# Optimization experiments

Measured on AMD Instinct MI355X. Metric: run time of the kernel, lower is better.

Reference implementation:

```python
import jax, jax.numpy as jnp
import numpy as np
from jax import lax

WIN = 9
LOSS_WEIGHT = 1.0

def _box_sum(x, win):
    return lax.reduce_window(x, 0.0, lax.add,
                             window_dimensions=(1, 1, win, win, win),
                             window_strides=(1, 1, 1, 1, 1),
                             padding='SAME')

def setup_inputs() -> dict:
    key = jax.random.key(0)
    k1, k2 = jax.random.split(key)
    shape = (2, 1, 160, 192, 160)
    predict = jax.random.uniform(k1, shape, dtype=jnp.float32)
    target = jax.random.uniform(k2, shape, dtype=jnp.float32)
    return {"predict": predict, "target": target}

def reference(predict, target):
    Ii, Ji = target, predict
    win = WIN
    win_size = float(win ** 3)

    I_sum = _box_sum(Ii, win)
    J_sum = _box_sum(Ji, win)
    I2_sum = _box_sum(Ii * Ii, win)
    J2_sum = _box_sum(Ji * Ji, win)
    IJ_sum = _box_sum(Ii * Ji, win)

    u_I = I_sum / win_size
    u_J = J_sum / win_size
    cross = IJ_sum - u_J * I_sum - u_I * J_sum + u_I * u_J * win_size
    I_var = I2_sum - 2.0 * u_I * I_sum + u_I * u_I * win_size
    J_var = J2_sum - 2.0 * u_J * J_sum + u_J * u_J * win_size
    cc = cross * cross / (I_var * J_var + 1e-05)
    loss = 1.0 - jnp.mean(cc)
    return loss * LOSS_WEIGHT
```

## Files before the change

kernel.cpp:

```cpp
#include <hip/hip_runtime.h>
#include <hip/hip_fp16.h>


#define NX 160
#define NY 192
#define NZ 160
#define NB 2
#define SLICE (NX * NY)
#define VOL   (SLICE * NZ)
#define TOTAL (VOL * NB)

#define TX 32
#define TY 16
#define ZC 8
#define GXT (NX / TX)
#define GYT (NY / TY)
#define GZT (NZ / ZC)
#define NBLK (GXT * GYT * GZT * NB)

#define HY 24
#define ZRS 56
#define ZQQ (HY * ZRS + 8)
#define RRS 40
#define RQQ (HY * RRS + 8)
#define SRS 40
#define SQQ (TY * SRS + 8)
#define INV729 (1.0f / 729.0f)

__device__ __forceinline__ void lds_barrier() {
    asm volatile("s_waitcnt lgkmcnt(0)" ::: "memory");
    __builtin_amdgcn_s_barrier();
}

__device__ __forceinline__ float4 f4add(float4 a, float4 b) {
    return make_float4(a.x + b.x, a.y + b.y, a.z + b.z, a.w + b.w);
}
__device__ __forceinline__ float4 f4sub(float4 a, float4 b) {
    return make_float4(a.x - b.x, a.y - b.y, a.z - b.z, a.w - b.w);
}
__device__ __forceinline__ float4 f4mul(float4 a, float4 b) {
    return make_float4(a.x * b.x, a.y * b.y, a.z * b.z, a.w * b.w);
}

union U8 { uint4 u; __half2 h[4]; };

__device__ __forceinline__ U8 ld8(const __half* p) {
    U8 r; r.u = *(const uint4*)p; return r;
}
__device__ __forceinline__ void st8(__half* p, const U8& v) {
    *(uint4*)p = v.u;
}

__global__ __launch_bounds__(256) void ncc_main(
    const float* __restrict__ J_pred,
    const float* __restrict__ I_targ,
    float* __restrict__ partial)
{
    const int tid = threadIdx.x;

    const int lin = blockIdx.x;
    const int s   = (lin & 7) * (NBLK / 8) + (lin >> 3);
    const int bx  = s % GXT;
    const int r1  = s / GXT;
    const int by  = r1 % GYT;
    const int r2  = r1 / GYT;
    const int zc  = r2 % GZT;
    const int b   = r2 / GZT;

    const int x0 = bx * TX;
    const int y0 = by * TY;
    const int z0 = zc * ZC;

    __shared__ __align__(16) __half Zq[5 * ZQQ];
    __shared__ __align__(16) __half Rq[5 * RQQ];
    __shared__ float redbuf[4];
    __half* const Sq = Zq;

    const bool is_col = (tid < 240);
    const int  crow = tid / 10;
    const int  cxg  = tid - crow * 10;
    const int  gy = y0 - 4 + crow;
    const int  gx = x0 - 4 + cxg * 4;
    const bool vxy = is_col && ((unsigned)gy < (unsigned)NY) && (gx >= 0) && (gx <= NX - 4);
    const size_t cbase = (size_t)b * VOL + (vxy ? (size_t)(gy * NX + gx) : 0);
    const float* const baseI = I_targ + cbase;
    const float* const baseJ = J_pred + cbase;

    const float4 f40 = make_float4(0.f, 0.f, 0.f, 0.f);
    float4 rS0 = f40, rS1 = f40, rS2 = f40, rS3 = f40, rS4 = f40;

#pragma unroll 3
    for (int ss = 0; ss < 9; ++ss) {
        const int z = z0 - 5 + ss;
        float4 aI = f40, aJ = f40;
        if (vxy && (unsigned)z < (unsigned)NZ) {
            aI = *(const float4*)(baseI + (size_t)z * SLICE);
            aJ = *(const float4*)(baseJ + (size_t)z * SLICE);
        }
        rS0 = f4add(rS0, aI);
        rS1 = f4add(rS1, aJ);
        rS2 = f4add(rS2, f4mul(aI, aI));
        rS3 = f4add(rS3, f4mul(aJ, aJ));
        rS4 = f4add(rS4, f4mul(aI, aJ));
    }

    float4 nIa = f40, nJa = f40, nIs = f40, nJs = f40;
    if (vxy) {
        const int za = z0 + 4;
        nIa = *(const float4*)(baseI + (size_t)za * SLICE);
        nJa = *(const float4*)(baseJ + (size_t)za * SLICE);
        const int zs = z0 - 5;
        if (zs >= 0) {
            nIs = *(const float4*)(baseI + (size_t)zs * SLICE);
            nJs = *(const float4*)(baseJ + (size_t)zs * SLICE);
        }
    }

    const int ty  = tid >> 4;
    const int tx2 = tid & 15;
    float acc = 0.f;

#pragma unroll 1
    for (int so = 0; so < ZC; ++so) {
        rS0 = f4add(rS0, f4sub(nIa, nIs));
        rS1 = f4add(rS1, f4sub(nJa, nJs));
        rS2 = f4add(rS2, f4sub(f4mul(nIa, nIa), f4mul(nIs, nIs)));
        rS3 = f4add(rS3, f4sub(f4mul(nJa, nJa), f4mul(nJs, nJs)));
        rS4 = f4add(rS4, f4sub(f4mul(nIa, nJa), f4mul(nIs, nJs)));

        nIa = f40; nJa = f40; nIs = f40; nJs = f40;
        if (so < ZC - 1 && vxy) {
            const int za = z0 + 5 + so;
            if (za < NZ) {
                nIa = *(const float4*)(baseI + (size_t)za * SLICE);
                nJa = *(const float4*)(baseJ + (size_t)za * SLICE);
            }
            const int zs = z0 + so - 4;
            if (zs >= 0) {
                nIs = *(const float4*)(baseI + (size_t)zs * SLICE);
                nJs = *(const float4*)(baseJ + (size_t)zs * SLICE);
            }
        }

        if (is_col) {
            const int o = crow * ZRS + cxg * 4;
            union { uint2 u; __half2 h[2]; } pk;
            pk.h[0] = __float22half2_rn(make_float2(rS0.x, rS0.y));
            pk.h[1] = __float22half2_rn(make_float2(rS0.z, rS0.w));
            *(uint2*)&Zq[0 * ZQQ + o] = pk.u;
            pk.h[0] = __float22half2_rn(make_float2(rS1.x, rS1.y));
            pk.h[1] = __float22half2_rn(make_float2(rS1.z, rS1.w));
            *(uint2*)&Zq[1 * ZQQ + o] = pk.u;
            pk.h[0] = __float22half2_rn(make_float2(rS2.x, rS2.y));
            pk.h[1] = __float22half2_rn(make_float2(rS2.z, rS2.w));
            *(uint2*)&Zq[2 * ZQQ + o] = pk.u;
            pk.h[0] = __float22half2_rn(make_float2(rS3.x, rS3.y));
            pk.h[1] = __float22half2_rn(make_float2(rS3.z, rS3.w));
            *(uint2*)&Zq[3 * ZQQ + o] = pk.u;
            pk.h[0] = __float22half2_rn(make_float2(rS4.x, rS4.y));
            pk.h[1] = __float22half2_rn(make_float2(rS4.z, rS4.w));
            *(uint2*)&Zq[4 * ZQQ + o] = pk.u;
        }
        lds_barrier();

        if (tid < 240) {
            const int q   = tid / 48;
            const int rem = tid - q * 48;
            const int row = rem >> 1;
            const int h   = rem & 1;
            const __half* src = &Zq[q * ZQQ + row * ZRS + h * 16];
            float c[24];
#pragma unroll
            for (int g = 0; g < 3; ++g) {
                U8 v = ld8(src + g * 8);
#pragma unroll
                for (int j = 0; j < 4; ++j) {
                    const float2 f = __half22float2(v.h[j]);
                    c[g * 8 + j * 2 + 0] = f.x;
                    c[g * 8 + j * 2 + 1] = f.y;
                }
            }
            float sx = c[0] + c[1] + c[2] + c[3] + c[4]
                     + c[5] + c[6] + c[7] + c[8];
            float o[16];
            o[0] = sx;
#pragma unroll
            for (int i = 1; i < 16; ++i) { sx += c[i + 8] - c[i - 1]; o[i] = sx; }
            __half* dst = &Rq[q * RQQ + row * RRS + h * 16];
#pragma unroll
            for (int g = 0; g < 2; ++g) {
                U8 w;
#pragma unroll
                for (int j = 0; j < 4; ++j)
                    w.h[j] = __float22half2_rn(make_float2(o[g * 8 + j * 2],
                                                           o[g * 8 + j * 2 + 1]));
                st8(dst + g * 8, w);
            }
        }
        lds_barrier();

        if (tid < 80) {
            const int q  = tid / 16;
            const int rm = tid & 15;
            const int xg = rm >> 2;
            const int q4 = rm & 3;
            const __half* rb = &Rq[q * RQQ + (q4 * 4) * RRS + xg * 8];
            __half* sb = &Sq[q * SQQ + (q4 * 4) * SRS + xg * 8];
            U8 sum = ld8(rb);
#pragma unroll
            for (int k = 1; k < 9; ++k) {
                const U8 t = ld8(rb + k * RRS);
#pragma unroll
                for (int j = 0; j < 4; ++j) sum.h[j] = __hadd2(sum.h[j], t.h[j]);
            }
            st8(sb, sum);
#pragma unroll
            for (int i = 1; i < 4; ++i) {
                const U8 nw = ld8(rb + (i + 8) * RRS);
                const U8 od = ld8(rb + (i - 1) * RRS);
#pragma unroll
                for (int j = 0; j < 4; ++j)
                    sum.h[j] = __hadd2(sum.h[j], __hsub2(nw.h[j], od.h[j]));
                st8(sb + i * SRS, sum);
            }
        }
        lds_barrier();

        {
            const int o = ty * SRS + tx2 * 2;
            const float2 S0 = __half22float2(*(const __half2*)&Sq[0 * SQQ + o]);
            const float2 S1 = __half22float2(*(const __half2*)&Sq[1 * SQQ + o]);
            const float2 S2 = __half22float2(*(const __half2*)&Sq[2 * SQQ + o]);
            const float2 S3 = __half22float2(*(const __half2*)&Sq[3 * SQQ + o]);
            const float2 S4 = __half22float2(*(const __half2*)&Sq[4 * SQQ + o]);
            {
                const float cross = S4.x - S0.x * S1.x * INV729;
                const float Iv    = S2.x - S0.x * S0.x * INV729;
                const float Jv    = S3.x - S1.x * S1.x * INV729;
                acc += (cross * cross) / (Iv * Jv + 1e-5f);
            }
            {
                const float cross = S4.y - S0.y * S1.y * INV729;
                const float Iv    = S2.y - S0.y * S0.y * INV729;
                const float Jv    = S3.y - S1.y * S1.y * INV729;
                acc += (cross * cross) / (Iv * Jv + 1e-5f);
            }
        }
        lds_barrier();
    }

#pragma unroll
    for (int off = 32; off > 0; off >>= 1) acc += __shfl_down(acc, off);
    __syncthreads();
    if ((tid & 63) == 0) redbuf[tid >> 6] = acc;
    __syncthreads();
    if (tid == 0) partial[s] = redbuf[0] + redbuf[1] + redbuf[2] + redbuf[3];
}

__global__ __launch_bounds__(256) void ncc_final(
    const float* __restrict__ partial, float* __restrict__ out)
{
    __shared__ float sm[256];
    const int tid = threadIdx.x;
    float v = 0.f;
    for (int i = tid; i < NBLK; i += 256) v += partial[i];
    sm[tid] = v;
    __syncthreads();
#pragma unroll
    for (int w = 128; w > 0; w >>= 1) {
        if (tid < w) sm[tid] += sm[tid + w];
        __syncthreads();
    }
    if (tid == 0) out[0] = 1.0f - sm[0] * (1.0f / (float)TOTAL);
}

extern "C" void kernel_launch(void* const* d_in, const int* in_sizes, int n_in,
                              void* d_out, int out_size, void* d_ws, size_t ws_size,
                              hipStream_t stream)
{
    const float* predict = (const float*)d_in[0];
    const float* target  = (const float*)d_in[1];
    float* partial = (float*)d_ws;

    ncc_main<<<dim3(NBLK), 256, 0, stream>>>(predict, target, partial);
    ncc_final<<<1, 256, 0, stream>>>(partial, (float*)d_out);
}
```

Before: 60.62 us.

## Use single-wavefront blocks with 16x16 tiles to drop workgroup barriers

Each block shrinks to one 64-lane wavefront that handles a 16x16 xy tile. Each lane now owns up to three halo columns, and the per-column z running sums are kept in registers. Because the block is a single wave, the s_barrier calls between LDS stages are replaced by lgkmcnt waits only, which removes workgroup synchronisation cost. In exchange the halo overhead per tile rises (24x24 halo for 16x16 outputs), which means more redundant global loads and more blocks. Register pressure also goes up from the 3x5 float4 running sums, and the loads are no longer prefetched a step ahead.

```diff
diff --git a/kernel.cpp b/kernel.cpp
--- a/kernel.cpp
+++ b/kernel.cpp
@@ -10,7 +10,7 @@
 #define VOL   (SLICE * NZ)
 #define TOTAL (VOL * NB)
 
-#define TX 32
+#define TX 16
 #define TY 16
 #define ZC 8
 #define GXT (NX / TX)
@@ -18,18 +18,17 @@
 #define GZT (NZ / ZC)
 #define NBLK (GXT * GYT * GZT * NB)
 
-#define HY 24
-#define ZRS 56
-#define ZQQ (HY * ZRS + 8)
-#define RRS 40
-#define RQQ (HY * RRS + 8)
-#define SRS 40
-#define SQQ (TY * SRS + 8)
+#define HR 24
+#define ZQS 24
+#define ZQQ (HR * ZQS + 8)
+#define RQS 24
+#define RQQ (HR * RQS + 8)
+#define SQS 16
+#define SQQ (TY * SQS + 8)
 #define INV729 (1.0f / 729.0f)
 
-__device__ __forceinline__ void lds_barrier() {
+__device__ __forceinline__ void lds_fence() {
     asm volatile("s_waitcnt lgkmcnt(0)" ::: "memory");
-    __builtin_amdgcn_s_barrier();
 }
 
 __device__ __forceinline__ float4 f4add(float4 a, float4 b) {
@@ -43,7 +42,6 @@
 }
 
 union U8 { uint4 u; __half2 h[4]; };
-
 __device__ __forceinline__ U8 ld8(const __half* p) {
     U8 r; r.u = *(const uint4*)p; return r;
 }
@@ -51,12 +49,12 @@
     *(uint4*)p = v.u;
 }
 
-__global__ __launch_bounds__(256) void ncc_main(
+__global__ __launch_bounds__(64) void ncc_main(
     const float* __restrict__ J_pred,
     const float* __restrict__ I_targ,
     float* __restrict__ partial)
 {
-    const int tid = threadIdx.x;
+    const int lane = threadIdx.x;
 
     const int lin = blockIdx.x;
     const int s   = (lin & 7) * (NBLK / 8) + (lin >> 3);
@@ -73,188 +71,195 @@
 
     __shared__ __align__(16) __half Zq[5 * ZQQ];
     __shared__ __align__(16) __half Rq[5 * RQQ];
-    __shared__ float redbuf[4];
-    __half* const Sq = Zq;
-
-    const bool is_col = (tid < 240);
-    const int  crow = tid / 10;
-    const int  cxg  = tid - crow * 10;
-    const int  gy = y0 - 4 + crow;
-    const int  gx = x0 - 4 + cxg * 4;
-    const bool vxy = is_col && ((unsigned)gy < (unsigned)NY) && (gx >= 0) && (gx <= NX - 4);
-    const size_t cbase = (size_t)b * VOL + (vxy ? (size_t)(gy * NX + gx) : 0);
-    const float* const baseI = I_targ + cbase;
-    const float* const baseJ = J_pred + cbase;
+    __shared__ __align__(16) __half Sq[5 * SQQ];
+
+    int  orow[3], oxg[3];
+    bool exist[3], ok[3];
+    const float* bI[3];
+    const float* bJ[3];
+    const size_t bvol = (size_t)b * VOL;
+#pragma unroll
+    for (int r = 0; r < 3; ++r) {
+        const int c = lane + r * 64;
+        exist[r] = (c < 144);
+        const int row = c / 6;
+        const int x   = c - row * 6;
+        orow[r] = row; oxg[r] = x;
+        const int gy = y0 - 4 + row;
+        const int gx = x0 - 4 + x * 4;
+        ok[r] = exist[r] && ((unsigned)gy < (unsigned)NY) && (gx >= 0) && (gx <= NX - 4);
+        const size_t cb = bvol + (ok[r] ? (size_t)(gy * NX + gx) : 0);
+        bI[r] = I_targ + cb;
+        bJ[r] = J_pred + cb;
+    }
 
     const float4 f40 = make_float4(0.f, 0.f, 0.f, 0.f);
-    float4 rS0 = f40, rS1 = f40, rS2 = f40, rS3 = f40, rS4 = f40;
-
-#pragma unroll 3
+    float4 run[3][5];
+#pragma unroll
+    for (int r = 0; r < 3; ++r)
+#pragma unroll
+        for (int q = 0; q < 5; ++q) run[r][q] = f40;
+
+#pragma unroll 1
     for (int ss = 0; ss < 9; ++ss) {
         const int z = z0 - 5 + ss;
-        float4 aI = f40, aJ = f40;
-        if (vxy && (unsigned)z < (unsigned)NZ) {
-            aI = *(const float4*)(baseI + (size_t)z * SLICE);
-            aJ = *(const float4*)(baseJ + (size_t)z * SLICE);
-        }
-        rS0 = f4add(rS0, aI);
-        rS1 = f4add(rS1, aJ);
-        rS2 = f4add(rS2, f4mul(aI, aI));
-        rS3 = f4add(rS3, f4mul(aJ, aJ));
-        rS4 = f4add(rS4, f4mul(aI, aJ));
-    }
-
-    float4 nIa = f40, nJa = f40, nIs = f40, nJs = f40;
-    if (vxy) {
-        const int za = z0 + 4;
-        nIa = *(const float4*)(baseI + (size_t)za * SLICE);
-        nJa = *(const float4*)(baseJ + (size_t)za * SLICE);
-        const int zs = z0 - 5;
-        if (zs >= 0) {
-            nIs = *(const float4*)(baseI + (size_t)zs * SLICE);
-            nJs = *(const float4*)(baseJ + (size_t)zs * SLICE);
-        }
-    }
-
-    const int ty  = tid >> 4;
-    const int tx2 = tid & 15;
+        const bool zok = ((unsigned)z < (unsigned)NZ);
+#pragma unroll
+        for (int r = 0; r < 3; ++r) {
+            float4 aI = f40, aJ = f40;
+            if (ok[r] && zok) {
+                aI = *(const float4*)(bI[r] + (size_t)z * SLICE);
+                aJ = *(const float4*)(bJ[r] + (size_t)z * SLICE);
+            }
+            run[r][0] = f4add(run[r][0], aI);
+            run[r][1] = f4add(run[r][1], aJ);
+            run[r][2] = f4add(run[r][2], f4mul(aI, aI));
+            run[r][3] = f4add(run[r][3], f4mul(aJ, aJ));
+            run[r][4] = f4add(run[r][4], f4mul(aI, aJ));
+        }
+    }
+
+    const int prow = lane >> 2;
+    const int pxq  = (lane & 3) * 4;
     float acc = 0.f;
 
 #pragma unroll 1
     for (int so = 0; so < ZC; ++so) {
-        rS0 = f4add(rS0, f4sub(nIa, nIs));
-        rS1 = f4add(rS1, f4sub(nJa, nJs));
-        rS2 = f4add(rS2, f4sub(f4mul(nIa, nIa), f4mul(nIs, nIs)));
-        rS3 = f4add(rS3, f4sub(f4mul(nJa, nJa), f4mul(nJs, nJs)));
-        rS4 = f4add(rS4, f4sub(f4mul(nIa, nJa), f4mul(nIs, nJs)));
-
-        nIa = f40; nJa = f40; nIs = f40; nJs = f40;
-        if (so < ZC - 1 && vxy) {
-            const int za = z0 + 5 + so;
-            if (za < NZ) {
-                nIa = *(const float4*)(baseI + (size_t)za * SLICE);
-                nJa = *(const float4*)(baseJ + (size_t)za * SLICE);
-            }
-            const int zs = z0 + so - 4;
-            if (zs >= 0) {
-                nIs = *(const float4*)(baseI + (size_t)zs * SLICE);
-                nJs = *(const float4*)(baseJ + (size_t)zs * SLICE);
-            }
-        }
-
-        if (is_col) {
-            const int o = crow * ZRS + cxg * 4;
-            union { uint2 u; __half2 h[2]; } pk;
-            pk.h[0] = __float22half2_rn(make_float2(rS0.x, rS0.y));
-            pk.h[1] = __float22half2_rn(make_float2(rS0.z, rS0.w));
-            *(uint2*)&Zq[0 * ZQQ + o] = pk.u;
-            pk.h[0] = __float22half2_rn(make_float2(rS1.x, rS1.y));
-            pk.h[1] = __float22half2_rn(make_float2(rS1.z, rS1.w));
-            *(uint2*)&Zq[1 * ZQQ + o] = pk.u;
-            pk.h[0] = __float22half2_rn(make_float2(rS2.x, rS2.y));
-            pk.h[1] = __float22half2_rn(make_float2(rS2.z, rS2.w));
-            *(uint2*)&Zq[2 * ZQQ + o] = pk.u;
-            pk.h[0] = __float22half2_rn(make_float2(rS3.x, rS3.y));
-            pk.h[1] = __float22half2_rn(make_float2(rS3.z, rS3.w));
-            *(uint2*)&Zq[3 * ZQQ + o] = pk.u;
-            pk.h[0] = __float22half2_rn(make_float2(rS4.x, rS4.y));
-            pk.h[1] = __float22half2_rn(make_float2(rS4.z, rS4.w));
-            *(uint2*)&Zq[4 * ZQQ + o] = pk.u;
-        }
-        lds_barrier();
-
-        if (tid < 240) {
-            const int q   = tid / 48;
-            const int rem = tid - q * 48;
-            const int row = rem >> 1;
-            const int h   = rem & 1;
-            const __half* src = &Zq[q * ZQQ + row * ZRS + h * 16];
-            float c[24];
-#pragma unroll
-            for (int g = 0; g < 3; ++g) {
-                U8 v = ld8(src + g * 8);
-#pragma unroll
-                for (int j = 0; j < 4; ++j) {
-                    const float2 f = __half22float2(v.h[j]);
-                    c[g * 8 + j * 2 + 0] = f.x;
-                    c[g * 8 + j * 2 + 1] = f.y;
-                }
-            }
-            float sx = c[0] + c[1] + c[2] + c[3] + c[4]
-                     + c[5] + c[6] + c[7] + c[8];
-            float o[16];
-            o[0] = sx;
-#pragma unroll
-            for (int i = 1; i < 16; ++i) { sx += c[i + 8] - c[i - 1]; o[i] = sx; }
-            __half* dst = &Rq[q * RQQ + row * RRS + h * 16];
-#pragma unroll
-            for (int g = 0; g < 2; ++g) {
-                U8 w;
-#pragma unroll
-                for (int j = 0; j < 4; ++j)
-                    w.h[j] = __float22half2_rn(make_float2(o[g * 8 + j * 2],
-                                                           o[g * 8 + j * 2 + 1]));
-                st8(dst + g * 8, w);
-            }
-        }
-        lds_barrier();
-
-        if (tid < 80) {
-            const int q  = tid / 16;
-            const int rm = tid & 15;
+        const int za = z0 + 4 + so;
+        const int zs = z0 + so - 5;
+        const bool zaok = ((unsigned)za < (unsigned)NZ);
+        const bool zsok = (zs >= 0);
+#pragma unroll
+        for (int r = 0; r < 3; ++r) {
+            float4 aI = f40, aJ = f40, sI = f40, sJ = f40;
+            if (ok[r]) {
+                if (zaok) {
+                    aI = *(const float4*)(bI[r] + (size_t)za * SLICE);
+                    aJ = *(const float4*)(bJ[r] + (size_t)za * SLICE);
+                }
+                if (zsok) {
+                    sI = *(const float4*)(bI[r] + (size_t)zs * SLICE);
+                    sJ = *(const float4*)(bJ[r] + (size_t)zs * SLICE);
+                }
+            }
+            run[r][0] = f4add(run[r][0], f4sub(aI, sI));
+            run[r][1] = f4add(run[r][1], f4sub(aJ, sJ));
+            run[r][2] = f4add(run[r][2], f4sub(f4mul(aI, aI), f4mul(sI, sI)));
+            run[r][3] = f4add(run[r][3], f4sub(f4mul(aJ, aJ), f4mul(sJ, sJ)));
+            run[r][4] = f4add(run[r][4], f4sub(f4mul(aI, aJ), f4mul(sI, sJ)));
+        }
+
+#pragma unroll
+        for (int r = 0; r < 3; ++r) {
+            if (exist[r]) {
+                const int o = orow[r] * ZQS + oxg[r] * 4;
+                union { uint2 u; __half2 h[2]; } pk;
+#pragma unroll
+                for (int q = 0; q < 5; ++q) {
+                    pk.h[0] = __float22half2_rn(make_float2(run[r][q].x, run[r][q].y));
+                    pk.h[1] = __float22half2_rn(make_float2(run[r][q].z, run[r][q].w));
+                    *(uint2*)&Zq[q * ZQQ + o] = pk.u;
+                }
+            }
+        }
+        lds_fence();
+
+#pragma unroll
+        for (int rr = 0; rr < 2; ++rr) {
+            const int t = lane + rr * 64;
+            if (t < 120) {
+                const int q   = t / 24;
+                const int row = t - q * 24;
+                const __half* src = &Zq[q * ZQQ + row * ZQS];
+                float c[24];
+#pragma unroll
+                for (int g = 0; g < 3; ++g) {
+                    U8 v = ld8(src + g * 8);
+#pragma unroll
+                    for (int j = 0; j < 4; ++j) {
+                        const float2 f = __half22float2(v.h[j]);
+                        c[g * 8 + j * 2 + 0] = f.x;
+                        c[g * 8 + j * 2 + 1] = f.y;
+                    }
+                }
+                float sx = c[0] + c[1] + c[2] + c[3] + c[4]
+                         + c[5] + c[6] + c[7] + c[8];
+                float o[16];
+                o[0] = sx;
+#pragma unroll
+                for (int i = 1; i < 16; ++i) { sx += c[i + 8] - c[i - 1]; o[i] = sx; }
+                __half* dst = &Rq[q * RQQ + row * RQS];
+#pragma unroll
+                for (int g = 0; g < 2; ++g) {
+                    U8 w;
+#pragma unroll
+                    for (int j = 0; j < 4; ++j)
+                        w.h[j] = __float22half2_rn(make_float2(o[g * 8 + j * 2],
+                                                               o[g * 8 + j * 2 + 1]));
+                    st8(dst + g * 8, w);
+                }
+            }
+        }
+        lds_fence();
+
+        if (lane < 40) {
+            const int q  = lane / 8;
+            const int rm = lane - q * 8;
             const int xg = rm >> 2;
             const int q4 = rm & 3;
-            const __half* rb = &Rq[q * RQQ + (q4 * 4) * RRS + xg * 8];
-            __half* sb = &Sq[q * SQQ + (q4 * 4) * SRS + xg * 8];
+            const __half* rb = &Rq[q * RQQ + (q4 * 4) * RQS + xg * 8];
+            __half* sb = &Sq[q * SQQ + (q4 * 4) * SQS + xg * 8];
             U8 sum = ld8(rb);
 #pragma unroll
             for (int k = 1; k < 9; ++k) {
-                const U8 t = ld8(rb + k * RRS);
+                const U8 t = ld8(rb + k * RQS);
 #pragma unroll
                 for (int j = 0; j < 4; ++j) sum.h[j] = __hadd2(sum.h[j], t.h[j]);
             }
             st8(sb, sum);
 #pragma unroll
             for (int i = 1; i < 4; ++i) {
-                const U8 nw = ld8(rb + (i + 8) * RRS);
-                const U8 od = ld8(rb + (i - 1) * RRS);
+                const U8 nw = ld8(rb + (i + 8) * RQS);
+                const U8 od = ld8(rb + (i - 1) * RQS);
 #pragma unroll
                 for (int j = 0; j < 4; ++j)
                     sum.h[j] = __hadd2(sum.h[j], __hsub2(nw.h[j], od.h[j]));
-                st8(sb + i * SRS, sum);
-            }
-        }
-        lds_barrier();
+                st8(sb + i * SQS, sum);
+            }
+        }
+        lds_fence();
 
         {
-            const int o = ty * SRS + tx2 * 2;
-            const float2 S0 = __half22float2(*(const __half2*)&Sq[0 * SQQ + o]);
-            const float2 S1 = __half22float2(*(const __half2*)&Sq[1 * SQQ + o]);
-            const float2 S2 = __half22float2(*(const __half2*)&Sq[2 * SQQ + o]);
-            const float2 S3 = __half22float2(*(const __half2*)&Sq[3 * SQQ + o]);
-            const float2 S4 = __half22float2(*(const __half2*)&Sq[4 * SQQ + o]);
-            {
-                const float cross = S4.x - S0.x * S1.x * INV729;
-                const float Iv    = S2.x - S0.x * S0.x * INV729;
-                const float Jv    = S3.x - S1.x * S1.x * INV729;
-                acc += (cross * cross) / (Iv * Jv + 1e-5f);
-            }
-            {
-                const float cross = S4.y - S0.y * S1.y * INV729;
-                const float Iv    = S2.y - S0.y * S0.y * INV729;
-                const float Jv    = S3.y - S1.y * S1.y * INV729;
-                acc += (cross * cross) / (Iv * Jv + 1e-5f);
-            }
-        }
-        lds_barrier();
+            const int o = prow * SQS + pxq;
+            union { uint2 u; __half2 h[2]; } v[5];
+#pragma unroll
+            for (int q = 0; q < 5; ++q) v[q].u = *(const uint2*)&Sq[q * SQQ + o];
+#pragma unroll
+            for (int j = 0; j < 2; ++j) {
+                const float2 S0 = __half22float2(v[0].h[j]);
+                const float2 S1 = __half22float2(v[1].h[j]);
+                const float2 S2 = __half22float2(v[2].h[j]);
+                const float2 S3 = __half22float2(v[3].h[j]);
+                const float2 S4 = __half22float2(v[4].h[j]);
+                {
+                    const float cross = S4.x - S0.x * S1.x * INV729;
+                    const float Iv    = S2.x - S0.x * S0.x * INV729;
+                    const float Jv    = S3.x - S1.x * S1.x * INV729;
+                    acc += (cross * cross) / (Iv * Jv + 1e-5f);
+                }
+                {
+                    const float cross = S4.y - S0.y * S1.y * INV729;
+                    const float Iv    = S2.y - S0.y * S0.y * INV729;
+                    const float Jv    = S3.y - S1.y * S1.y * INV729;
+                    acc += (cross * cross) / (Iv * Jv + 1e-5f);
+                }
+            }
+        }
     }
 
 #pragma unroll
     for (int off = 32; off > 0; off >>= 1) acc += __shfl_down(acc, off);
-    __syncthreads();
-    if ((tid & 63) == 0) redbuf[tid >> 6] = acc;
-    __syncthreads();
-    if (tid == 0) partial[s] = redbuf[0] + redbuf[1] + redbuf[2] + redbuf[3];
+    if (lane == 0) partial[s] = acc;
 }
 
 __global__ __launch_bounds__(256) void ncc_final(
@@ -282,6 +287,6 @@
     const float* target  = (const float*)d_in[1];
     float* partial = (float*)d_ws;
 
-    ncc_main<<<dim3(NBLK), 256, 0, stream>>>(predict, target, partial);
+    ncc_main<<<dim3(NBLK), 64, 0, stream>>>(predict, target, partial);
     ncc_final<<<1, 256, 0, stream>>>(partial, (float*)d_out);
 }
```

After: 77.98 us. +28.6%, slower.

## Replace Y-direction box sum and final stage with bf16 MFMA band-matrix multiply

Applied to the files above, without the earlier changes.

The Y-direction 9-tap sliding sum over half-precision rows is replaced by a bf16 MFMA against a constant banded 0/1 weight matrix. The X-pass output is stored as bf16 in a transposed layout and read with ds_read_b64_tr_b16. The NCC epilogue now consumes the MFMA accumulators directly, which removes one LDS stage and one barrier per z-slice. The z-loop is software-pipelined so the MFMA/epilogue of the previous slice overlaps the global loads for the next. Risks include lower bf16 precision in the X-pass sums and only two waves doing the MFMA work.

```diff
diff --git a/kernel.cpp b/kernel.cpp
--- a/kernel.cpp
+++ b/kernel.cpp
@@ -18,20 +18,32 @@
 #define GZT (NZ / ZC)
 #define NBLK (GXT * GYT * GZT * NB)
 
-#define HY 24
-#define ZRS 56
-#define ZQQ (HY * ZRS + 8)
-#define RRS 40
-#define RQQ (HY * RRS + 8)
-#define SRS 40
-#define SQQ (TY * SRS + 8)
+#define HR 24
+#define ZQS 48
+#define ZQQ (HR * ZQS + 8)
+#define RGN 544
 #define INV729 (1.0f / 729.0f)
+
+typedef short bf16x8 __attribute__((ext_vector_type(8)));
+typedef float f32x4 __attribute__((ext_vector_type(4)));
 
 __device__ __forceinline__ void lds_barrier() {
     asm volatile("s_waitcnt lgkmcnt(0)" ::: "memory");
     __builtin_amdgcn_s_barrier();
 }
 
+__device__ __forceinline__ unsigned cvt_pk_bf16(float lo, float hi) {
+    unsigned r;
+    asm("v_cvt_pk_bf16_f32 %0, %1, %2" : "=v"(r) : "v"(lo), "v"(hi));
+    return r;
+}
+
+__device__ __forceinline__ uint2 tr_rd(unsigned a) {
+    uint2 d;
+    asm volatile("ds_read_b64_tr_b16 %0, %1" : "=v"(d) : "v"(a));
+    return d;
+}
+
 __device__ __forceinline__ float4 f4add(float4 a, float4 b) {
     return make_float4(a.x + b.x, a.y + b.y, a.z + b.z, a.w + b.w);
 }
@@ -43,12 +55,8 @@
 }
 
 union U8 { uint4 u; __half2 h[4]; };
-
 __device__ __forceinline__ U8 ld8(const __half* p) {
     U8 r; r.u = *(const uint4*)p; return r;
-}
-__device__ __forceinline__ void st8(__half* p, const U8& v) {
-    *(uint4*)p = v.u;
 }
 
 __global__ __launch_bounds__(256) void ncc_main(
@@ -72,9 +80,14 @@
     const int z0 = zc * ZC;
 
     __shared__ __align__(16) __half Zq[5 * ZQQ];
-    __shared__ __align__(16) __half Rq[5 * RQQ];
+    __shared__ __align__(16) short  RqT[10 * RGN];
     __shared__ float redbuf[4];
-    __half* const Sq = Zq;
+
+    if (tid < 160) {
+        const int r = tid >> 4, slot = tid & 15;
+        const int e = (slot < 8) ? (192 + slot * 8) : (448 + (slot - 8) * 8);
+        *(uint4*)&RqT[r * RGN + e] = make_uint4(0, 0, 0, 0);
+    }
 
     const bool is_col = (tid < 240);
     const int  crow = tid / 10;
@@ -86,10 +99,23 @@
     const float* const baseI = I_targ + cbase;
     const float* const baseJ = J_pred + cbase;
 
+    const int lane = tid & 63;
+    bf16x8 wfrag;
+    {
+        const int m = lane & 15, kb = (lane >> 4) * 8;
+#pragma unroll
+        for (int j = 0; j < 8; ++j) {
+            const int k = kb + j;
+            wfrag[j] = (k >= m && k <= m + 8) ? (short)0x3F80 : (short)0;
+        }
+    }
+    const unsigned rqbase = (unsigned)(size_t)&RqT[0];
+    const unsigned trlane = rqbase + 2u * (unsigned)(lane & 15) + 128u * (unsigned)(lane >> 4);
+
     const float4 f40 = make_float4(0.f, 0.f, 0.f, 0.f);
     float4 rS0 = f40, rS1 = f40, rS2 = f40, rS3 = f40, rS4 = f40;
 
-#pragma unroll 3
+#pragma unroll 1
     for (int ss = 0; ss < 9; ++ss) {
         const int z = z0 - 5 + ss;
         float4 aI = f40, aJ = f40;
@@ -104,46 +130,17 @@
         rS4 = f4add(rS4, f4mul(aI, aJ));
     }
 
-    float4 nIa = f40, nJa = f40, nIs = f40, nJs = f40;
+    float4 nIa = f40, nJa = f40;
     if (vxy) {
-        const int za = z0 + 4;
-        nIa = *(const float4*)(baseI + (size_t)za * SLICE);
-        nJa = *(const float4*)(baseJ + (size_t)za * SLICE);
-        const int zs = z0 - 5;
-        if (zs >= 0) {
-            nIs = *(const float4*)(baseI + (size_t)zs * SLICE);
-            nJs = *(const float4*)(baseJ + (size_t)zs * SLICE);
-        }
-    }
-
-    const int ty  = tid >> 4;
-    const int tx2 = tid & 15;
+        nIa = *(const float4*)(baseI + (size_t)(z0 + 4) * SLICE);
+        nJa = *(const float4*)(baseJ + (size_t)(z0 + 4) * SLICE);
+    }
+
     float acc = 0.f;
 
-#pragma unroll 1
-    for (int so = 0; so < ZC; ++so) {
-        rS0 = f4add(rS0, f4sub(nIa, nIs));
-        rS1 = f4add(rS1, f4sub(nJa, nJs));
-        rS2 = f4add(rS2, f4sub(f4mul(nIa, nIa), f4mul(nIs, nIs)));
-        rS3 = f4add(rS3, f4sub(f4mul(nJa, nJa), f4mul(nJs, nJs)));
-        rS4 = f4add(rS4, f4sub(f4mul(nIa, nJa), f4mul(nIs, nJs)));
-
-        nIa = f40; nJa = f40; nIs = f40; nJs = f40;
-        if (so < ZC - 1 && vxy) {
-            const int za = z0 + 5 + so;
-            if (za < NZ) {
-                nIa = *(const float4*)(baseI + (size_t)za * SLICE);
-                nJa = *(const float4*)(baseJ + (size_t)za * SLICE);
-            }
-            const int zs = z0 + so - 4;
-            if (zs >= 0) {
-                nIs = *(const float4*)(baseI + (size_t)zs * SLICE);
-                nJs = *(const float4*)(baseJ + (size_t)zs * SLICE);
-            }
-        }
-
+    auto do_P1 = [&]() {
         if (is_col) {
-            const int o = crow * ZRS + cxg * 4;
+            const int o = crow * ZQS + cxg * 4;
             union { uint2 u; __half2 h[2]; } pk;
             pk.h[0] = __float22half2_rn(make_float2(rS0.x, rS0.y));
             pk.h[1] = __float22half2_rn(make_float2(rS0.z, rS0.w));
@@ -161,14 +158,15 @@
             pk.h[1] = __float22half2_rn(make_float2(rS4.z, rS4.w));
             *(uint2*)&Zq[4 * ZQQ + o] = pk.u;
         }
-        lds_barrier();
-
+    };
+
+    auto do_P2 = [&]() {
         if (tid < 240) {
             const int q   = tid / 48;
             const int rem = tid - q * 48;
             const int row = rem >> 1;
             const int h   = rem & 1;
-            const __half* src = &Zq[q * ZQQ + row * ZRS + h * 16];
+            const __half* src = &Zq[q * ZQQ + row * ZQS + h * 16];
             float c[24];
 #pragma unroll
             for (int g = 0; g < 3; ++g) {
@@ -186,68 +184,101 @@
             o[0] = sx;
 #pragma unroll
             for (int i = 1; i < 16; ++i) { sx += c[i + 8] - c[i - 1]; o[i] = sx; }
-            __half* dst = &Rq[q * RQQ + row * RRS + h * 16];
-#pragma unroll
-            for (int g = 0; g < 2; ++g) {
-                U8 w;
-#pragma unroll
-                for (int j = 0; j < 4; ++j)
-                    w.h[j] = __float22half2_rn(make_float2(o[g * 8 + j * 2],
-                                                           o[g * 8 + j * 2 + 1]));
-                st8(dst + g * 8, w);
+            unsigned u[8];
+#pragma unroll
+            for (int i = 0; i < 8; ++i) u[i] = cvt_pk_bf16(o[2 * i], o[2 * i + 1]);
+            const int e = 16 * (row & 3) + 64 * (row >> 3) + 256 * ((row >> 2) & 1);
+            short* dst = &RqT[(q * 2 + h) * RGN + e];
+            *(uint4*)(dst + 0) = make_uint4(u[0], u[1], u[2], u[3]);
+            *(uint4*)(dst + 8) = make_uint4(u[4], u[5], u[6], u[7]);
+        }
+    };
+
+    auto do_mfmacc = [&]() {
+        if (tid < 128) {
+            const int h = tid >> 6;
+            const unsigned abase = trlane + (unsigned)h * 1088u;
+            const f32x4 z4 = {0.f, 0.f, 0.f, 0.f};
+            f32x4 D[5];
+#pragma unroll
+            for (int q = 0; q < 5; ++q) {
+                const unsigned a = abase + (unsigned)q * 2176u;
+                uint2 b0 = tr_rd(a);
+                uint2 b1 = tr_rd(a + 512u);
+                asm volatile("s_waitcnt lgkmcnt(0)" ::: "memory");
+                __builtin_amdgcn_sched_barrier(0);
+                union { uint2 u[2]; bf16x8 v; } bb;
+                bb.u[0] = b0; bb.u[1] = b1;
+                D[q] = __builtin_amdgcn_mfma_f32_16x16x32_bf16(wfrag, bb.v, z4, 0, 0, 0);
             }
-        }
-        lds_barrier();
-
-        if (tid < 80) {
-            const int q  = tid / 16;
-            const int rm = tid & 15;
-            const int xg = rm >> 2;
-            const int q4 = rm & 3;
-            const __half* rb = &Rq[q * RQQ + (q4 * 4) * RRS + xg * 8];
-            __half* sb = &Sq[q * SQQ + (q4 * 4) * SRS + xg * 8];
-            U8 sum = ld8(rb);
-#pragma unroll
-            for (int k = 1; k < 9; ++k) {
-                const U8 t = ld8(rb + k * RRS);
-#pragma unroll
-                for (int j = 0; j < 4; ++j) sum.h[j] = __hadd2(sum.h[j], t.h[j]);
-            }
-            st8(sb, sum);
-#pragma unroll
-            for (int i = 1; i < 4; ++i) {
-                const U8 nw = ld8(rb + (i + 8) * RRS);
-                const U8 od = ld8(rb + (i - 1) * RRS);
-#pragma unroll
-                for (int j = 0; j < 4; ++j)
-                    sum.h[j] = __hadd2(sum.h[j], __hsub2(nw.h[j], od.h[j]));
-                st8(sb + i * SRS, sum);
-            }
-        }
-        lds_barrier();
-
-        {
-            const int o = ty * SRS + tx2 * 2;
-            const float2 S0 = __half22float2(*(const __half2*)&Sq[0 * SQQ + o]);
-            const float2 S1 = __half22float2(*(const __half2*)&Sq[1 * SQQ + o]);
-            const float2 S2 = __half22float2(*(const __half2*)&Sq[2 * SQQ + o]);
-            const float2 S3 = __half22float2(*(const __half2*)&Sq[3 * SQQ + o]);
-            const float2 S4 = __half22float2(*(const __half2*)&Sq[4 * SQQ + o]);
-            {
-                const float cross = S4.x - S0.x * S1.x * INV729;
-                const float Iv    = S2.x - S0.x * S0.x * INV729;
-                const float Jv    = S3.x - S1.x * S1.x * INV729;
+#pragma unroll
+            for (int r = 0; r < 4; ++r) {
+                const float S0 = D[0][r], S1 = D[1][r], S2 = D[2][r],
+                            S3 = D[3][r], S4 = D[4][r];
+                const float cross = S4 - S0 * S1 * INV729;
+                const float Iv    = S2 - S0 * S0 * INV729;
+                const float Jv    = S3 - S1 * S1 * INV729;
                 acc += (cross * cross) / (Iv * Jv + 1e-5f);
             }
-            {
-                const float cross = S4.y - S0.y * S1.y * INV729;
-                const float Iv    = S2.y - S0.y * S0.y * INV729;
-                const float Jv    = S3.y - S1.y * S1.y * INV729;
-                acc += (cross * cross) / (Iv * Jv + 1e-5f);
+        }
+    };
+
+    {
+        float4 sI = f40, sJ = f40;
+        const int zs = z0 - 5;
+        if (vxy && zs >= 0) {
+            sI = *(const float4*)(baseI + (size_t)zs * SLICE);
+            sJ = *(const float4*)(baseJ + (size_t)zs * SLICE);
+        }
+        rS0 = f4add(rS0, f4sub(nIa, sI));
+        rS1 = f4add(rS1, f4sub(nJa, sJ));
+        rS2 = f4add(rS2, f4sub(f4mul(nIa, nIa), f4mul(sI, sI)));
+        rS3 = f4add(rS3, f4sub(f4mul(nJa, nJa), f4mul(sJ, sJ)));
+        rS4 = f4add(rS4, f4sub(f4mul(nIa, nJa), f4mul(sI, sJ)));
+        nIa = f40; nJa = f40;
+        if (vxy) {
+            nIa = *(const float4*)(baseI + (size_t)(z0 + 5) * SLICE);
+            nJa = *(const float4*)(baseJ + (size_t)(z0 + 5) * SLICE);
+        }
+        do_P1();
+        lds_barrier();
+        do_P2();
+        lds_barrier();
+    }
+
+#pragma unroll 1
+    for (int t = 0; t < ZC - 1; ++t) {
+        const int ss = t + 1;
+        float4 sI = f40, sJ = f40;
+        const int zs = z0 + ss - 5;
+        if (vxy && zs >= 0) {
+            sI = *(const float4*)(baseI + (size_t)zs * SLICE);
+            sJ = *(const float4*)(baseJ + (size_t)zs * SLICE);
+        }
+
+        do_mfmacc();
+
+        rS0 = f4add(rS0, f4sub(nIa, sI));
+        rS1 = f4add(rS1, f4sub(nJa, sJ));
+        rS2 = f4add(rS2, f4sub(f4mul(nIa, nIa), f4mul(sI, sI)));
+        rS3 = f4add(rS3, f4sub(f4mul(nJa, nJa), f4mul(sJ, sJ)));
+        rS4 = f4add(rS4, f4sub(f4mul(nIa, nJa), f4mul(sI, sJ)));
+        nIa = f40; nJa = f40;
+        if (ss < ZC - 1 && vxy) {
+            const int za = z0 + 5 + ss;
+            if (za < NZ) {
+                nIa = *(const float4*)(baseI + (size_t)za * SLICE);
+                nJa = *(const float4*)(baseJ + (size_t)za * SLICE);
             }
         }
+
+        do_P1();
         lds_barrier();
-    }
+        do_P2();
+        lds_barrier();
+    }
+
+    do_mfmacc();
 
 #pragma unroll
     for (int off = 32; off > 0; off >>= 1) acc += __shfl_down(acc, off);
```

Measured after the change: 61.23 us, median of 4. Within noise of the previous version (+1.0%).
